# Kernel tuning notes

Hardware: AMD Instinct MI355X
Metric: run time of the kernel (lower is better)

The kernel has to match this reference:

```python
import jax, jax.numpy as jnp
import numpy as np

EPS = 1e-5
DILATIONS = (1, 2, 1, 2, 1, 2, 1, 2)   # 4 blocks x 2 layers, kernel_size=2
GCN_AT = {1: 0, 5: 1}                  # ChebConv applied before layers 1 and 5
N_NODES, T_IN, N_EDGES = 20000, 13, 200000
RC, DC, SC, EC, HORIZON = 32, 32, 256, 512, 12


def conv_1x1(x, W, b):
    # x: [N,C,T], W: [O,C] -> [N,O,T]
    return jnp.einsum('oc,nct->not', W, x) + b[None, :, None]


def conv_k2(x, W, b, d):
    # dilated conv, kernel=2, dilation=d. x: [N,C,T], W: [O,C,2] -> [N,O,T-d]
    y = jnp.einsum('oc,nct->not', W[:, :, 0], x[:, :, :-d]) \
        + jnp.einsum('oc,nct->not', W[:, :, 1], x[:, :, d:])
    return y + b[None, :, None]


def _batchnorm(x):
    # BatchNorm2d (train mode, gamma=1, beta=0); per-channel stats over (N, F=1, T)
    m = jnp.mean(x, axis=(0, 2), keepdims=True)
    v = jnp.var(x, axis=(0, 2), keepdims=True)
    return (x - m) / jnp.sqrt(v + EPS)


def _cheb(xf, edge_index, edge_attr, W0, W1, b):
    n = xf.shape[0]
    row, col = edge_index[0], edge_index[1]
    w = jnp.where(row == col, 0.0, edge_attr)               # remove_self_loops
    deg = jax.ops.segment_sum(w, row, num_segments=n)
    dinv = jnp.where(deg > 0, 1.0 / jnp.sqrt(jnp.where(deg > 0, deg, 1.0)), 0.0)
    norm = dinv[row] * w * dinv[col]                        # [E]
    tx1 = -jax.ops.segment_sum(norm[:, None] * xf[row], col, num_segments=n)
    return xf @ W0 + tx1 @ W1 + b


def _forward(x, edge_index, edge_attr, start_W, start_b, filter_W, filter_b,
             gate_W, gate_b, skip_W, skip_b, gcn0_W0, gcn0_W1, gcn0_b,
             gcn1_W0, gcn1_W1, gcn1_b, end1_W, end1_b, end2_W, end2_b):
    # instance norm over time (use_norm=True); means is detached in torch
    means = jax.lax.stop_gradient(jnp.mean(x, axis=1, keepdims=True))   # [N,1,1]
    xc = x - means
    stdev = jnp.sqrt(jnp.var(xc, axis=1, keepdims=True) + EPS)
    xc = xc / stdev
    h = xc[:, :, 0][:, None, :]                  # [N,1,13]  (F=1 dim folded away)
    h = conv_1x1(h, start_W, start_b)            # [N,32,13]; T == receptive_field, no pad
    gcns = ((gcn0_W0, gcn0_W1, gcn0_b), (gcn1_W0, gcn1_W1, gcn1_b))
    skip = None
    for i, d in enumerate(DILATIONS):
        if i in GCN_AT:
            n, c, t = h.shape
            W0, W1, b = gcns[GCN_AT[i]]
            h = _cheb(h.reshape(n, c * t), edge_index, edge_attr, W0, W1, b).reshape(n, c, t)
        residual = h
        f = jnp.tanh(conv_k2(residual, filter_W[i], filter_b[i], d))
        g = jax.nn.sigmoid(conv_k2(residual, gate_W[i], gate_b[i], d))
        h = f * g                                 # [N,32,t-d]
        s = conv_1x1(h, skip_W[i], skip_b[i])     # [N,256,t-d]
        skip = s if skip is None else s + skip[:, :, -s.shape[2]:]
        h = h + residual[:, :, -h.shape[2]:]      # residual add (residual_conv unused in source)
        h = _batchnorm(h)
    out = jax.nn.relu(skip)                       # [N,256,1]
    out = conv_1x1(out, end1_W, end1_b)           # [N,512,1]
    out = conv_1x1(out, end2_W, end2_b)           # [N,12,1]
    return out * stdev + means                    # de-normalize; broadcasts over horizon


def setup_inputs() -> dict:
    key = jax.random.key(0)
    ks = iter(jax.random.split(key, 32))
    def w(shape, scale=0.1):
        return jax.random.normal(next(ks), shape, dtype=jnp.float32) * scale
    return {
        'x': jax.random.normal(next(ks), (N_NODES, T_IN, 1), dtype=jnp.float32),
        'edge_index': jax.random.randint(next(ks), (2, N_EDGES), 0, N_NODES),
        'edge_attr': jax.random.uniform(next(ks), (N_EDGES,), dtype=jnp.float32),
        'start_W': w((RC, 1)), 'start_b': w((RC,)),
        'filter_W': w((8, DC, RC, 2)), 'filter_b': w((8, DC)),
        'gate_W': w((8, DC, RC, 2)), 'gate_b': w((8, DC)),
        'skip_W': w((8, SC, DC)), 'skip_b': w((8, SC)),
        'gcn0_W0': w((384, 384), 0.05), 'gcn0_W1': w((384, 384), 0.05), 'gcn0_b': w((384,)),
        'gcn1_W0': w((192, 192), 0.05), 'gcn1_W1': w((192, 192), 0.05), 'gcn1_b': w((192,)),
        'end1_W': w((EC, SC)), 'end1_b': w((EC,)),
        'end2_W': w((HORIZON, EC)), 'end2_b': w((HORIZON,)),
    }


def reference(x, edge_index, edge_attr, start_W, start_b, filter_W, filter_b,
              gate_W, gate_b, skip_W, skip_b, gcn0_W0, gcn0_W1, gcn0_b,
              gcn1_W0, gcn1_W1, gcn1_b, end1_W, end1_b, end2_W, end2_b):
    return _forward(x, edge_index, edge_attr, start_W, start_b, filter_W, filter_b,
                    gate_W, gate_b, skip_W, skip_b, gcn0_W0, gcn0_W1, gcn0_b,
                    gcn1_W0, gcn1_W1, gcn1_b, end1_W, end1_b, end2_W, end2_b)
```

## Files before the change

### kernel.cpp

```cpp
#include <hip/hip_runtime.h>
#include <math.h>

#define NN 20000
#define NE 200000
#define TT 13
#define NBLK 79

typedef short bf16x8 __attribute__((ext_vector_type(8)));
typedef float f32x4 __attribute__((ext_vector_type(4)));

__device__ inline unsigned short f2bf(float f){
  union{float f; unsigned u;} v; v.f = f;
  unsigned r = v.u + 0x7fffu + ((v.u >> 16) & 1u);
  return (unsigned short)(r >> 16);
}
__device__ inline float bf2f(unsigned short h){
  union{unsigned u; float f;} v; v.u = ((unsigned)h) << 16; return v.f;
}
__device__ inline float fsig(float x){ return __builtin_amdgcn_rcpf(1.f + __expf(-x)); }
__device__ inline float ftanh(float x){ return 2.f*__builtin_amdgcn_rcpf(1.f + __expf(-2.f*x)) - 1.f; }

__device__ inline void d_prepw2(const float* W0, const float* W1, const float* b,
    unsigned short* Wt, float* bPerm, int F, int Kp, int T, int idx){
  if(idx >= F*Kp) return;
// ... 26 lines not shown
  if(c == 0){
    float b = e2b[k];
    for(int o = 0; o < 512; o++) b += e2W[k*512+o]*e1b[o];
    bc[k] = b;
  }
}
__device__ inline void d_prepg(const float* fW, const float* fb,
    const float* gW, const float* gb, unsigned short* Wfrag, float* Bfrag, int idx){
  if(idx < 8*8*64*8){
    int j = idx & 7; int lane = (idx >> 3) & 63; int chunk = (idx >> 9) & 7; int layer = idx >> 12;
    int fg = chunk >> 2; int q = (chunk >> 1) & 1; int i = chunk & 1;
    int quad = lane >> 4, tcol = lane & 15;
    int cout = 16*i + tcol, cin = quad*8 + j;
    const float* W = fg ? gW : fW;
    Wfrag[idx] = f2bf(W[layer*2048 + cout*64 + cin*2 + q]);
  }
  if(idx < 8*64*4){
    int r = idx & 3; int lane = (idx >> 2) & 63; int layer = idx >> 8;
    int tcol = lane & 15;
    float v;
    if(r == 0)      v = fb[layer*32 + tcol];
    else if(r == 1) v = fb[layer*32 + 16 + tcol];
    else if(r == 2) v = gb[layer*32 + tcol];
    else            v = gb[layer*32 + 16 + tcol];
    Bfrag[idx] = v;
  }
}
__global__ __launch_bounds__(256) void k_prepall(
    const float* g0W0, const float* g0W1, const float* g0b,
    const float* g1W0, const float* g1W1, const float* g1b,
    const float* sW, const float* sb,
    const float* e1W, const float* e1b, const float* e2W, const float* e2b,
    const float* fW, const float* fb, const float* gW, const float* gb,
    unsigned short* Wt0, float* bP0, unsigned short* Wt1, float* bP1,
    unsigned short* Bwt, float* bias2, float* Wc, float* bc,
    unsigned short* Wfrag, float* Bfrag){
  int b = blockIdx.x, t = threadIdx.x;
  if(b < 1152)       d_prepw2(g0W0, g0W1, g0b, Wt0, bP0, 384, 768, 12, b*256 + t);
  else if(b < 1440)  d_prepw2(g1W0, g1W1, g1b, Wt1, bP1, 192, 384, 6, (b-1152)*256 + t);
  else if(b < 1696)  d_prep2(sW, sb, Bwt, bias2, (b-1440)*256 + t);
  else if(b < 1708)  d_comb(e1W, e1b, e2W, e2b, Wc, bc, (b-1696)*256 + t);
  else               d_prepg(fW, fb, gW, gb, Wfrag, Bfrag, (b-1708)*256 + t);
}

__global__ __launch_bounds__(256) void k_deg(const int* __restrict__ ei,
    const float* __restrict__ ea, float* __restrict__ deg){
  int e = blockIdx.x*256 + threadIdx.x;
  if(e >= NE) return;
  int r = ei[e], c = ei[NE+e];
  float w = (r==c) ? 0.f : ea[e];
  if(w != 0.f) atomicAdd(&deg[r], w);
}

__global__ __launch_bounds__(256) void k_dinv(float* __restrict__ deg){
  int n = blockIdx.x*256 + threadIdx.x;
  if(n >= NN) return;
  float d = deg[n];
  deg[n] = (d > 0.f) ? rsqrtf(d) : 0.f;
}

__global__ __launch_bounds__(256) void k_normcount(const int* __restrict__ ei,
    const float* __restrict__ ea, const float* __restrict__ dinv,
    float* __restrict__ nrm, int* __restrict__ cnt){
  int e = blockIdx.x*256 + threadIdx.x;
  if(e >= NE) return;
  int r = ei[e], c = ei[NE+e];
  float w = (r==c) ? 0.f : ea[e];
  float nv = dinv[r]*w*dinv[c];
  nrm[e] = nv;
  if(nv != 0.f) atomicAdd(&cnt[c], 1);
}

__global__ __launch_bounds__(256) void k_scanA(const int* __restrict__ cnt, int* __restrict__ bsum){
  int i = blockIdx.x*256 + threadIdx.x;
  int l = threadIdx.x & 63, w = threadIdx.x >> 6;
  int v = (i < NN) ? cnt[i] : 0;
#pragma unroll
  for(int off = 1; off < 64; off <<= 1) v += __shfl_xor(v, off);
  __shared__ int ws4[4];
  if(l == 0) ws4[w] = v;
  __syncthreads();
  if(threadIdx.x == 0) bsum[blockIdx.x] = ws4[0]+ws4[1]+ws4[2]+ws4[3];
}

__global__ __launch_bounds__(256) void k_scanC(const int* __restrict__ cnt,
    const int* __restrict__ bsum, int* __restrict__ rowptr, int* __restrict__ woff){
  __shared__ int sb[128];
  int t = threadIdx.x;
  if(t < 128) sb[t] = (t < NBLK) ? bsum[t] : 0;
  __syncthreads();
  for(int off = 1; off < 128; off <<= 1){
    int u = 0;
    if(t < 128 && t >= off) u = sb[t-off];
    __syncthreads();
    if(t < 128) sb[t] += u;
    __syncthreads();
  }
  int i = blockIdx.x*256 + t;
  int l = t & 63, w = t >> 6;
  int v = (i < NN) ? cnt[i] : 0;
  int x = v;
#pragma unroll
  for(int off = 1; off < 64; off <<= 1){
    int u = __shfl_up(x, off);
    if(l >= off) x += u;
  }
  __shared__ int wt[4];
  if(l == 63) wt[w] = x;
  __syncthreads();
  int wo = 0;
  for(int k = 0; k < w; k++) wo += wt[k];
  int bb = (blockIdx.x > 0) ? sb[blockIdx.x-1] : 0;
  int excl = bb + wo + x - v;
  if(i < NN){ rowptr[i] = excl; woff[i] = excl; }
  if(i == 0) rowptr[NN] = sb[NBLK-1];
}

__global__ __launch_bounds__(256) void k_place(const float* __restrict__ nrm,
    const int* __restrict__ ei, int* __restrict__ woff,
    int* __restrict__ rowArr, float* __restrict__ nrmArr){
  int e = blockIdx.x*256 + threadIdx.x;
  if(e >= NE) return;
  float nv = nrm[e];
  if(nv == 0.f) return;
  int c = ei[NE+e];
  int pos = atomicAdd(&woff[c], 1);
  rowArr[pos] = ei[e];
  nrmArr[pos] = nv;
}

__global__ void k_gather3(const unsigned short* __restrict__ h, int F, int F2,
    const float* __restrict__ bnstats, float cntInv,
    const int* __restrict__ rowArr, const float* __restrict__ nrmArr,
    const int* __restrict__ rowptr, unsigned short* __restrict__ tx1){
  __shared__ float bnm[32], bnv[32];
  __shared__ int srow[64];
  __shared__ float snrm[64];
  int tid = threadIdx.x;
  if(tid < 32){
    float s = 0.f, s2 = 0.f;
#pragma unroll
    for(int b = 0; b < 16; b++){ s += bnstats[b*64 + tid]; s2 += bnstats[b*64 + 32 + tid]; }
    float m = s*cntInv; float var = s2*cntInv - m*m;
    bnm[tid] = m; bnv[tid] = rsqrtf(var + 1e-5f);
  }
  __syncthreads();
  int node = blockIdx.x;
  int f2 = tid;
  int c0 = (2*f2) & 31;
  float m0 = bnm[c0], i0 = bnv[c0], m1 = bnm[c0+1], i1 = bnv[c0+1];
  int beg = rowptr[node], end = rowptr[node+1];
  float a0 = 0.f, a1 = 0.f;
  for(int base = beg; base < end; base += 64){
    int m = end - base; if(m > 64) m = 64;
    __syncthreads();
    if(tid < m){ srow[tid] = rowArr[base+tid]; snrm[tid] = nrmArr[base+tid]; }
    __syncthreads();
    if(f2 < F2){
      for(int j = 0; j < m; j++){
        unsigned u = *(const unsigned*)(h + (size_t)srow[j]*F + 2*f2);
        float nv = snrm[j];
        a0 += nv*(bf2f((unsigned short)(u & 0xffffu)) - m0)*i0;
        a1 += nv*(bf2f((unsigned short)(u >> 16)) - m1)*i1;
      }
    }
  }
  if(f2 < F2){
    unsigned outw = (unsigned)f2bf(-a0) | ((unsigned)f2bf(-a1) << 16);
    *(unsigned*)(tx1 + (size_t)node*F + 2*f2) = outw;
  }
}

template<bool BOUT>
__global__ __launch_bounds__(256) void k_gemm_gcn(
    const unsigned short* __restrict__ hSrc, const unsigned short* __restrict__ tx1,
    const unsigned short* __restrict__ Bt, const float* __restrict__ bias,
    const float* __restrict__ bnstats, float cntInv,
    void* __restrict__ Cv, int M, int N, int F){
  __shared__ unsigned short As[128*32];
  __shared__ unsigned short Bs[64*32];
  __shared__ float bnm[32], bnv[32];
  int tid = threadIdx.x;
  if(tid < 32){
    float s = 0.f, s2 = 0.f;
#pragma unroll
    for(int b = 0; b < 16; b++){ s += bnstats[b*64 + tid]; s2 += bnstats[b*64 + 32 + tid]; }
    float m = s*cntInv; float var = s2*cntInv - m*m;
    bnm[tid] = m; bnv[tid] = rsqrtf(var + 1e-5f);
  }
  __syncthreads();
  int w = tid >> 6, l = tid & 63, quad = l >> 4, tcol = l & 15;
  int m0 = blockIdx.x*128, n0 = blockIdx.y*64;
  int rw = (w & 1)*64, cw = (w >> 1)*32;
  int sr = tid >> 2, sc = (tid & 3)*8;
  float am[8], ai[8];
#pragma unroll
  for(int j = 0; j < 8; j++){ am[j] = bnm[sc+j]; ai[j] = bnv[sc+j]; }
  int K = 2*F;
  f32x4 acc[4][2];
#pragma unroll
  for(int i = 0; i < 4; i++)
#pragma unroll
    for(int j = 0; j < 2; j++) acc[i][j] = (f32x4){0.f,0.f,0.f,0.f};
  for(int k0 = 0; k0 < K; k0 += 32){
    uint4 a0r, a1r;
    if(k0 < F){
      uint4 r0 = *(const uint4*)(hSrc + (size_t)(m0 + sr)*F + k0 + sc);
      uint4 r1 = *(const uint4*)(hSrc + (size_t)(m0 + 64 + sr)*F + k0 + sc);
      unsigned short o0[8], o1[8];
      const unsigned short* p0 = (const unsigned short*)&r0;
      const unsigned short* p1 = (const unsigned short*)&r1;
#pragma unroll
      for(int j = 0; j < 8; j++){
        o0[j] = f2bf((bf2f(p0[j]) - am[j])*ai[j]);
        o1[j] = f2bf((bf2f(p1[j]) - am[j])*ai[j]);
      }
      a0r = *(const uint4*)o0; a1r = *(const uint4*)o1;
    } else {
      a0r = *(const uint4*)(tx1 + (size_t)(m0 + sr)*F + (k0-F) + sc);
      a1r = *(const uint4*)(tx1 + (size_t)(m0 + 64 + sr)*F + (k0-F) + sc);
    }
    uint4 b0 = *(const uint4*)(Bt + (size_t)(n0 + sr)*K + k0 + sc);
    __syncthreads();
    *(uint4*)(As + sr*32 + sc) = a0r;
    *(uint4*)(As + (64+sr)*32 + sc) = a1r;
    *(uint4*)(Bs + sr*32 + sc) = b0;
    __syncthreads();
    bf16x8 av[4], bv[2];
#pragma unroll
    for(int i = 0; i < 4; i++) av[i] = *(const bf16x8*)(As + (rw + 16*i + tcol)*32 + quad*8);
#pragma unroll
    for(int j = 0; j < 2; j++) bv[j] = *(const bf16x8*)(Bs + (cw + 16*j + tcol)*32 + quad*8);
#pragma unroll
    for(int i = 0; i < 4; i++)
#pragma unroll
      for(int j = 0; j < 2; j++)
        acc[i][j] = __builtin_amdgcn_mfma_f32_16x16x32_bf16(av[i], bv[j], acc[i][j], 0, 0, 0);
  }
#pragma unroll
  for(int i = 0; i < 4; i++){
#pragma unroll
    for(int j = 0; j < 2; j++){
      int col = n0 + cw + 16*j + tcol;
      float bb = bias[col];
#pragma unroll
      for(int r = 0; r < 4; r++){
        int row = m0 + rw + 16*i + quad*4 + r;
        if(row < M){
          float o = acc[i][j][r] + bb;
          if(BOUT) ((unsigned short*)Cv)[(size_t)row*N + col] = f2bf(o);
          else ((float*)Cv)[(size_t)row*N + col] = o;
        }
      }
    }
  }
}

template<bool BOUT>
__global__ __launch_bounds__(256) void k_gemm_bf16(const unsigned short* __restrict__ A,
    const unsigned short* __restrict__ Bt, const float* __restrict__ bias,
    void* __restrict__ Cv, int M, int N, int K){
  __shared__ unsigned short As[128*32];
  __shared__ unsigned short Bs[64*32];
  int tid = threadIdx.x;
  int w = tid >> 6, l = tid & 63, quad = l >> 4, tcol = l & 15;
  int m0 = blockIdx.x*128, n0 = blockIdx.y*64;
  int rw = (w & 1)*64, cw = (w >> 1)*32;
  int sr = tid >> 2, sc = (tid & 3)*8;
  f32x4 acc[4][2];
#pragma unroll
  for(int i = 0; i < 4; i++)
#pragma unroll
    for(int j = 0; j < 2; j++) acc[i][j] = (f32x4){0.f,0.f,0.f,0.f};
  for(int k0 = 0; k0 < K; k0 += 32){
    uint4 a0 = *(const uint4*)(A + (size_t)(m0 + sr)*K + k0 + sc);
    uint4 a1 = *(const uint4*)(A + (size_t)(m0 + 64 + sr)*K + k0 + sc);
    uint4 b0 = *(const uint4*)(Bt + (size_t)(n0 + sr)*K + k0 + sc);
    __syncthreads();
    *(uint4*)(As + sr*32 + sc) = a0;
    *(uint4*)(As + (64+sr)*32 + sc) = a1;
    *(uint4*)(Bs + sr*32 + sc) = b0;
    __syncthreads();
    bf16x8 av[4], bv[2];
#pragma unroll
    for(int i = 0; i < 4; i++) av[i] = *(const bf16x8*)(As + (rw + 16*i + tcol)*32 + quad*8);
#pragma unroll
    for(int j = 0; j < 2; j++) bv[j] = *(const bf16x8*)(Bs + (cw + 16*j + tcol)*32 + quad*8);
#pragma unroll
    for(int i = 0; i < 4; i++)
#pragma unroll
      for(int j = 0; j < 2; j++)
        acc[i][j] = __builtin_amdgcn_mfma_f32_16x16x32_bf16(av[i], bv[j], acc[i][j], 0, 0, 0);
  }
#pragma unroll
  for(int i = 0; i < 4; i++){
#pragma unroll
    for(int j = 0; j < 2; j++){
      int col = n0 + cw + 16*j + tcol;
      float bb = bias[col];
#pragma unroll
      for(int r = 0; r < 4; r++){
        int row = m0 + rw + 16*i + quad*4 + r;
        if(row < M){
          float o = acc[i][j][r] + bb;
          if(BOUT) ((unsigned short*)Cv)[(size_t)row*N + col] = f2bf(o);
          else ((float*)Cv)[(size_t)row*N + col] = o;
        }
      }
    }
  }
}

__global__ __launch_bounds__(256,3) void k_fused0nb(
    const float* __restrict__ x, const float* __restrict__ startW, const float* __restrict__ startb,
    const unsigned short* __restrict__ Wfrag, const float* __restrict__ Bfrag,
    unsigned short* __restrict__ glcat, unsigned short* __restrict__ hOut,
    float* __restrict__ stdev, float* __restrict__ means,
    float* __restrict__ bnstats){
  __shared__ float xs[40][14];
  __shared__ float swl[32], sbl[32];
  __shared__ unsigned short bufB[40*12*40];
  __shared__ float bnred[64];
  int tid = threadIdx.x;
  int w = tid >> 6, l = tid & 63, quad = l >> 4, tcol = l & 15;
  int base = blockIdx.x*40;
  for(int j = tid; j < 520; j += 256){ int n = j/13, t = j - n*13; xs[n][t] = x[(size_t)(base+n)*13 + t]; }
  if(tid < 32){ swl[tid] = startW[tid]; sbl[tid] = startb[tid]; }
  if(tid < 64) bnred[tid] = 0.f;
  __syncthreads();
  if(tid < 40){
    float s = 0.f;
#pragma unroll
    for(int t = 0; t < 13; t++) s += xs[tid][t];
    float m = s*(1.0f/13.f);
    float s2 = 0.f;
#pragma unroll
    for(int t = 0; t < 13; t++){ float d = xs[tid][t]-m; s2 += d*d; }
    float sd = sqrtf(s2*(1.0f/13.f) + 1e-5f);
    float inv = 1.0f/sd;
    means[base+tid] = m; stdev[base+tid] = sd;
#pragma unroll
    for(int t = 0; t < 13; t++) xs[tid][t] = (xs[tid][t]-m)*inv;
  }
  __syncthreads();
  bf16x8 bwf[2][2], bwg[2][2];
#pragma unroll
  for(int q = 0; q < 2; q++)
#pragma unroll
    for(int i = 0; i < 2; i++){
      bwf[q][i] = *(const bf16x8*)(Wfrag + ((q*2+i)*64 + l)*8);
      bwg[q][i] = *(const bf16x8*)(Wfrag + ((4 + q*2+i)*64 + l)*8);
    }
  float4 bv4 = *(const float4*)(Bfrag + l*4);
  float fbv[2] = {bv4.x, bv4.y}, gbv[2] = {bv4.z, bv4.w};
  float sw8[8], sb8[8], swc[2], sbc[2];
#pragma unroll
  for(int j = 0; j < 8; j++){ sw8[j] = swl[quad*8+j]; sb8[j] = sbl[quad*8+j]; }
#pragma unroll
  for(int i = 0; i < 2; i++){ swc[i] = swl[16*i+tcol]; sbc[i] = sbl[16*i+tcol]; }
  float sAc[2] = {0.f,0.f}, s2Ac[2] = {0.f,0.f};
  int tr = (tcol < 12) ? tcol : 0;
  for(int p = 0; p < 5; p++){
    int slA = w*10 + 2*p, slB = slA + 1;
// ... 169 lines not shown
      agA[i] = __builtin_amdgcn_mfma_f32_16x16x32_bf16(aA0, bwg[0][i], agA[i], 0,0,0);
      agB[i] = __builtin_amdgcn_mfma_f32_16x16x32_bf16(aB0, bwg[0][i], agB[i], 0,0,0);
      agA[i] = __builtin_amdgcn_mfma_f32_16x16x32_bf16(aA1, bwg[1][i], agA[i], 0,0,0);
      agB[i] = __builtin_amdgcn_mfma_f32_16x16x32_bf16(aB1, bwg[1][i], agB[i], 0,0,0);
    }
#pragma unroll
    for(int i=0;i<2;i++){
      int cout = 16*i + tcol;
#pragma unroll
      for(int r=0;r<4;r++){
        int t = quad*4 + r;
        if(t < TOUT){
          float fA = afA[i][r] + fbv[i];
          float gA = agA[i][r] + gbv[i];
          float fB = afB[i][r] + fbv[i];
          float gB = agB[i][r] + gbv[i];
          float gatedA = ftanh(fA)*fsig(gA);
          float gatedB = ftanh(fB)*fsig(gB);
          if(t == TOUT-1){
            gl[(size_t)nA*256 + cout] = f2bf(gatedA);
            gl[(size_t)nB*256 + cout] = f2bf(gatedB);
          }
          float oA = gatedA + bf2f(hwA[(t+D)*RS + cout]);
          float oB = gatedB + bf2f(hwB[(t+D)*RS + cout]);
          if(WRITEH){ howA[t*RS + cout] = f2bf(oA); howB[t*RS + cout] = f2bf(oB); }
          if(STATS){ sA[i] += oA + oB; s2A[i] += oA*oA + oB*oB; }
        }
      }
    }
    if(WRITEH && l < TOUT*4){
      int to = l >> 2, cb2 = (l & 3)*8;
      *(uint4*)(hOut + (size_t)nA*TOUT*32 + to*32 + cb2) = *(const uint4*)(howA + to*RS + cb2);
      *(uint4*)(hOut + (size_t)nB*TOUT*32 + to*32 + cb2) = *(const uint4*)(howB + to*RS + cb2);
    }
  }
  if(STATS){
#pragma unroll
    for(int i=0;i<2;i++){
      sA[i]  += __shfl_xor(sA[i], 16);  sA[i]  += __shfl_xor(sA[i], 32);
      s2A[i] += __shfl_xor(s2A[i], 16); s2A[i] += __shfl_xor(s2A[i], 32);
    }
    if(l < 16){
#pragma unroll
      for(int i=0;i<2;i++){
        atomicAdd(&bnred[16*i + l], sA[i]);
        atomicAdd(&bnred[32 + 16*i + l], s2A[i]);
      }
    }
    __syncthreads();
    if(tid < 64) atomicAdd(&bnOut[(blockIdx.x & 15)*64 + tid], bnred[tid]);
  }
}

__global__ __launch_bounds__(256) void k_final(const float* __restrict__ skip,
    const float* __restrict__ Wc, const float* __restrict__ bc,
    const float* __restrict__ stdev, const float* __restrict__ means,
    float* __restrict__ out){
  __shared__ float wsm[3072];
  __shared__ float bcs[12];
  int tid = threadIdx.x;
  for(int j = tid; j < 3072; j += 256){
    int c = j / 12, k = j - c*12;
    wsm[c*12 + k] = Wc[k*256 + c];
  }
  if(tid < 12) bcs[tid] = bc[tid];
  __syncthreads();
  int idx = blockIdx.x*256 + tid;
  if(idx >= NN*12) return;
  int n = idx / 12, k = idx - n*12;
  const float* sr = skip + (size_t)n*256;
  float acc = bcs[k];
#pragma unroll 8
  for(int c = 0; c < 256; c++) acc += wsm[c*12 + k]*fmaxf(sr[c], 0.f);
  out[idx] = acc*stdev[n] + means[n];
}

extern "C" void kernel_launch(void* const* d_in, const int* in_sizes, int n_in,
                              void* d_out, int out_size, void* d_ws, size_t ws_size,
                              hipStream_t stream) {
  const float* x      = (const float*)d_in[0];
  const int*   ei     = (const int*)  d_in[1];
  const float* ea     = (const float*)d_in[2];
  const float* startW = (const float*)d_in[3];
  const float* startb = (const float*)d_in[4];
  const float* fW     = (const float*)d_in[5];
  const float* fb     = (const float*)d_in[6];
  const float* gW     = (const float*)d_in[7];
  const float* gb     = (const float*)d_in[8];
  const float* sW     = (const float*)d_in[9];
  const float* sb     = (const float*)d_in[10];
  const float* g0W0   = (const float*)d_in[11];
  const float* g0W1   = (const float*)d_in[12];
  const float* g0b    = (const float*)d_in[13];
  const float* g1W0   = (const float*)d_in[14];
  const float* g1W1   = (const float*)d_in[15];
  const float* g1b    = (const float*)d_in[16];
  const float* e1W    = (const float*)d_in[17];
  const float* e1b    = (const float*)d_in[18];
  const float* e2W    = (const float*)d_in[19];
  const float* e2b    = (const float*)d_in[20];
  float* out = (float*)d_out;
  float* ws  = (float*)d_ws;

  const int MP = 20096;
  size_t o = 0;
  float* hAf = ws + o; o += (size_t)NN*208;
  float* hBf = ws + o; o += (size_t)NN*208;
  unsigned short* hA = (unsigned short*)hAf;
  unsigned short* hB = (unsigned short*)hBf;
  unsigned short* tx1   = (unsigned short*)(ws + o); o += (size_t)MP*192;
  unsigned short* glcat = (unsigned short*)(ws + o); o += (size_t)MP*128;
  unsigned short* Wt0 = (unsigned short*)(ws + o); o += 147456;
  unsigned short* Wt1 = (unsigned short*)(ws + o); o += 36864;
  unsigned short* Bwt = (unsigned short*)(ws + o); o += 32768;
  unsigned short* Wfrag = (unsigned short*)(ws + o); o += 16384;
  float* Bfrag = ws + o; o += 2048;
  float* bP0   = ws + o; o += 384;
  float* bP1   = ws + o; o += 192;
  float* bias2 = ws + o; o += 256;
  float* Wc    = ws + o; o += 3072;
  float* bc    = ws + o; o += 16;
  float* stdev = ws + o; o += NN;
  float* means = ws + o; o += NN;
  float* deg   = ws + o; o += NN;
  int*   cnt   = (int*)(ws + o); o += NN;
  float* bnstats = ws + o; o += 8*1024;
  float* normb = ws + o; o += NE;
  int*   rowArr = (int*)(ws + o); o += NE;
  float* nrmArr = ws + o; o += NE;
  int*   rowptr = (int*)(ws + o); o += NN + 4;
  int*   woff   = (int*)(ws + o); o += NN;
  int*   bsum   = (int*)(ws + o); o += NBLK + 4;
  float* skipb  = hAf;

  hipMemsetAsync(deg, 0, (size_t)(2*NN + 8*1024)*sizeof(float), stream);
  k_prepall<<<1836, 256, 0, stream>>>(g0W0, g0W1, g0b, g1W0, g1W1, g1b,
      sW, sb, e1W, e1b, e2W, e2b, fW, fb, gW, gb,
      Wt0, bP0, Wt1, bP1, Bwt, bias2, Wc, bc, Wfrag, Bfrag);
  k_deg<<<(NE+255)/256, 256, 0, stream>>>(ei, ea, deg);
  k_dinv<<<(NN+255)/256, 256, 0, stream>>>(deg);
  k_normcount<<<(NE+255)/256, 256, 0, stream>>>(ei, ea, deg, normb, cnt);
  k_scanA<<<NBLK, 256, 0, stream>>>(cnt, bsum);
  k_scanC<<<NBLK, 256, 0, stream>>>(cnt, bsum, rowptr, woff);
  k_place<<<(NE+255)/256, 256, 0, stream>>>(normb, ei, woff, rowArr, nrmArr);

  const int GB = 1280;
  k_fused0nb<<<500, 256, 0, stream>>>(x, startW, startb, Wfrag, Bfrag, glcat, hB,
      stdev, means, bnstats);
  k_gather3<<<NN, 192, 0, stream>>>(hB, 384, 192, bnstats, 1.f/(NN*12.f),
      rowArr, nrmArr, rowptr, tx1);
  { dim3 g(MP/128, 384/64);
    k_gemm_gcn<true><<<g, 256, 0, stream>>>(hB, tx1, Wt0, bP0, bnstats, 1.f/(NN*12.f),
        hA, NN, 384, 384); }
  k_gated5<2,12,10,false,true,true><<<GB,256,0,stream>>>(hA, hB, glcat+32,
      bnstats, bnstats+1*1024, Wfrag, Bfrag, 1, 0.f);
  k_gated5<1,10,9,true,true,true><<<GB,256,0,stream>>>(hB, hA, glcat+64,
      bnstats+1*1024, bnstats+2*1024, Wfrag, Bfrag, 2, 1.f/(NN*10.f));
  k_gated5<2,9,7,true,true,true><<<GB,256,0,stream>>>(hA, hB, glcat+96,
      bnstats+2*1024, bnstats+3*1024, Wfrag, Bfrag, 3, 1.f/(NN*9.f));
  k_gated5<1,7,6,true,true,true><<<GB,256,0,stream>>>(hB, hA, glcat+128,
      bnstats+3*1024, bnstats+4*1024, Wfrag, Bfrag, 4, 1.f/(NN*7.f));
  k_gather3<<<NN, 128, 0, stream>>>(hA, 192, 96, bnstats+4*1024, 1.f/(NN*6.f),
      rowArr, nrmArr, rowptr, tx1);
  { dim3 g(MP/128, 192/64);
    k_gemm_gcn<true><<<g, 256, 0, stream>>>(hA, tx1, Wt1, bP1, bnstats+4*1024, 1.f/(NN*6.f),
        hB, NN, 192, 192); }
  k_gated5<2,6,4,false,true,true><<<GB,256,0,stream>>>(hB, hA, glcat+160,
      bnstats, bnstats+5*1024, Wfrag, Bfrag, 5, 0.f);
  k_gated5<1,4,3,true,true,true><<<GB,256,0,stream>>>(hA, hB, glcat+192,
      bnstats+5*1024, bnstats+6*1024, Wfrag, Bfrag, 6, 1.f/(NN*4.f));
  k_gated5<2,3,1,true,false,false><<<GB,256,0,stream>>>(hB, nullptr, glcat+224,
      bnstats+6*1024, bnstats+7*1024, Wfrag, Bfrag, 7, 1.f/(NN*3.f));

  { dim3 g(MP/128, 256/64);
    k_gemm_bf16<false><<<g, 256, 0, stream>>>(glcat, Bwt, bias2, skipb, NN, 256, 256); }
  k_final<<<((NN*12)+255)/256, 256, 0, stream>>>(skipb, Wc, bc, stdev, means, out);
}
```

Before: 432.8 us.

## Fuse GCN GEMM with following gated layer and skip GEMM with final head

Replaces the standalone ChebConv GEMM and the next gated TCN layer with one kernel. It keeps the 32-node GCN output tile in shared memory, runs the dilated filter/gate MFMAs on it and accumulates the batch-norm statistics there. It also fuses the skip GEMM with the ReLU and end-projection head so the fp32 skip buffer is never written out, and folds the dinv kernel into normcount. This removes intermediate global round-trips and several launches. In exchange the fused GCN kernel uses narrow 32-row tiles that reload the full weight matrix per block, with large shared memory and possibly lower occupancy.

```diff
diff --git a/kernel.cpp b/kernel.cpp
--- a/kernel.cpp
+++ b/kernel.cpp
@@ -102,21 +102,17 @@
   if(w != 0.f) atomicAdd(&deg[r], w);
 }
 
-__global__ __launch_bounds__(256) void k_dinv(float* __restrict__ deg){
-  int n = blockIdx.x*256 + threadIdx.x;
-  if(n >= NN) return;
-  float d = deg[n];
-  deg[n] = (d > 0.f) ? rsqrtf(d) : 0.f;
-}
-
 __global__ __launch_bounds__(256) void k_normcount(const int* __restrict__ ei,
-    const float* __restrict__ ea, const float* __restrict__ dinv,
+    const float* __restrict__ ea, const float* __restrict__ deg,
     float* __restrict__ nrm, int* __restrict__ cnt){
   int e = blockIdx.x*256 + threadIdx.x;
   if(e >= NE) return;
   int r = ei[e], c = ei[NE+e];
   float w = (r==c) ? 0.f : ea[e];
-  float nv = dinv[r]*w*dinv[c];
+  float dr = deg[r], dc = deg[c];
+  float ir = (dr > 0.f) ? rsqrtf(dr) : 0.f;
+  float ic = (dc > 0.f) ? rsqrtf(dc) : 0.f;
+  float nv = ir*w*ic;
   nrm[e] = nv;
   if(nv != 0.f) atomicAdd(&cnt[c], 1);
 }
@@ -221,16 +217,22 @@
   }
 }
 
-template<bool BOUT>
-__global__ __launch_bounds__(256) void k_gemm_gcn(
+template<int F,int TIN,int TOUT,int D,int NCT>
+__global__ __launch_bounds__(256) void k_gcn_gated(
     const unsigned short* __restrict__ hSrc, const unsigned short* __restrict__ tx1,
-    const unsigned short* __restrict__ Bt, const float* __restrict__ bias,
+    const unsigned short* __restrict__ Bt, const float* __restrict__ biasP,
     const float* __restrict__ bnstats, float cntInv,
-    void* __restrict__ Cv, int M, int N, int F){
-  __shared__ unsigned short As[128*32];
-  __shared__ unsigned short Bs[64*32];
+    const unsigned short* __restrict__ Wfrag, const float* __restrict__ Bfrag, int layer,
+    unsigned short* __restrict__ gl, unsigned short* __restrict__ hOut,
+    float* __restrict__ bnOut){
+  constexpr int RS = 40;
+  constexpr int SH = (F*32 > 32*TIN*RS) ? F*32 : 32*TIN*RS;
+  __shared__ unsigned short shm[SH];
+  __shared__ unsigned short As[32*32];
   __shared__ float bnm[32], bnv[32];
+  __shared__ float bnred[64];
   int tid = threadIdx.x;
+  int w = tid >> 6, l = tid & 63, quad = l >> 4, tcol = l & 15;
   if(tid < 32){
     float s = 0.f, s2 = 0.f;
 #pragma unroll
@@ -238,127 +240,155 @@
     float m = s*cntInv; float var = s2*cntInv - m*m;
     bnm[tid] = m; bnv[tid] = rsqrtf(var + 1e-5f);
   }
-  __syncthreads();
-  int w = tid >> 6, l = tid & 63, quad = l >> 4, tcol = l & 15;
-  int m0 = blockIdx.x*128, n0 = blockIdx.y*64;
-  int rw = (w & 1)*64, cw = (w >> 1)*32;
-  int sr = tid >> 2, sc = (tid & 3)*8;
+  if(tid < 64) bnred[tid] = 0.f;
+  __syncthreads();
+  int m0 = blockIdx.x*32;
   float am[8], ai[8];
-#pragma unroll
-  for(int j = 0; j < 8; j++){ am[j] = bnm[sc+j]; ai[j] = bnv[sc+j]; }
-  int K = 2*F;
-  f32x4 acc[4][2];
-#pragma unroll
-  for(int i = 0; i < 4; i++)
-#pragma unroll
-    for(int j = 0; j < 2; j++) acc[i][j] = (f32x4){0.f,0.f,0.f,0.f};
+  {
+    int off8 = (tid & 3)*8;
+#pragma unroll
+    for(int j = 0; j < 8; j++){ am[j] = bnm[off8+j]; ai[j] = bnv[off8+j]; }
+  }
+  constexpr int NB4 = F*4/256;
+  f32x4 acc[2][NCT];
+#pragma unroll
+  for(int i = 0; i < 2; i++)
+#pragma unroll
+    for(int j = 0; j < NCT; j++) acc[i][j] = (f32x4){0.f,0.f,0.f,0.f};
+  const int K = 2*F;
   for(int k0 = 0; k0 < K; k0 += 32){
-    uint4 a0r, a1r;
-    if(k0 < F){
-      uint4 r0 = *(const uint4*)(hSrc + (size_t)(m0 + sr)*F + k0 + sc);
-      uint4 r1 = *(const uint4*)(hSrc + (size_t)(m0 + 64 + sr)*F + k0 + sc);
-      unsigned short o0[8], o1[8];
-      const unsigned short* p0 = (const unsigned short*)&r0;
-      const unsigned short* p1 = (const unsigned short*)&r1;
-#pragma unroll
-      for(int j = 0; j < 8; j++){
-        o0[j] = f2bf((bf2f(p0[j]) - am[j])*ai[j]);
-        o1[j] = f2bf((bf2f(p1[j]) - am[j])*ai[j]);
+    uint4 a4 = {0,0,0,0};
+    if(tid < 128){
+      int row = tid >> 2, off = (tid & 3)*8;
+      if(k0 < F){
+        uint4 r0 = *(const uint4*)(hSrc + (size_t)(m0+row)*F + k0 + off);
+        unsigned short o0[8];
+        const unsigned short* p0 = (const unsigned short*)&r0;
+#pragma unroll
+        for(int j = 0; j < 8; j++) o0[j] = f2bf((bf2f(p0[j]) - am[j])*ai[j]);
+        a4 = *(const uint4*)o0;
+      } else {
+        a4 = *(const uint4*)(tx1 + (size_t)(m0+row)*F + (k0-F) + off);
       }
-      a0r = *(const uint4*)o0; a1r = *(const uint4*)o1;
-    } else {
-      a0r = *(const uint4*)(tx1 + (size_t)(m0 + sr)*F + (k0-F) + sc);
-      a1r = *(const uint4*)(tx1 + (size_t)(m0 + 64 + sr)*F + (k0-F) + sc);
-    }
-    uint4 b0 = *(const uint4*)(Bt + (size_t)(n0 + sr)*K + k0 + sc);
+    }
+    uint4 b4[NB4];
+#pragma unroll
+    for(int it = 0; it < NB4; it++){
+      int idx = tid + 256*it;
+      b4[it] = *(const uint4*)(Bt + (size_t)(idx>>2)*K + k0 + (idx&3)*8);
+    }
     __syncthreads();
-    *(uint4*)(As + sr*32 + sc) = a0r;
-    *(uint4*)(As + (64+sr)*32 + sc) = a1r;
-    *(uint4*)(Bs + sr*32 + sc) = b0;
+    if(tid < 128) *(uint4*)(As + (tid>>2)*32 + (tid&3)*8) = a4;
+#pragma unroll
+    for(int it = 0; it < NB4; it++){
+      int idx = tid + 256*it;
+      *(uint4*)(shm + (idx>>2)*32 + (idx&3)*8) = b4[it];
+    }
     __syncthreads();
-    bf16x8 av[4], bv[2];
-#pragma unroll
-    for(int i = 0; i < 4; i++) av[i] = *(const bf16x8*)(As + (rw + 16*i + tcol)*32 + quad*8);
-#pragma unroll
-    for(int j = 0; j < 2; j++) bv[j] = *(const bf16x8*)(Bs + (cw + 16*j + tcol)*32 + quad*8);
-#pragma unroll
-    for(int i = 0; i < 4; i++)
-#pragma unroll
-      for(int j = 0; j < 2; j++)
+    bf16x8 av[2], bv[NCT];
+#pragma unroll
+    for(int i = 0; i < 2; i++) av[i] = *(const bf16x8*)(As + (16*i + tcol)*32 + quad*8);
+#pragma unroll
+    for(int j = 0; j < NCT; j++) bv[j] = *(const bf16x8*)(shm + ((w*NCT + j)*16 + tcol)*32 + quad*8);
+#pragma unroll
+    for(int i = 0; i < 2; i++)
+#pragma unroll
+      for(int j = 0; j < NCT; j++)
         acc[i][j] = __builtin_amdgcn_mfma_f32_16x16x32_bf16(av[i], bv[j], acc[i][j], 0, 0, 0);
   }
-#pragma unroll
-  for(int i = 0; i < 4; i++){
-#pragma unroll
-    for(int j = 0; j < 2; j++){
-      int col = n0 + cw + 16*j + tcol;
-      float bb = bias[col];
+  __syncthreads();
+  unsigned short* hs = shm;
+#pragma unroll
+  for(int i = 0; i < 2; i++)
+#pragma unroll
+    for(int j = 0; j < NCT; j++){
+      int col = (w*NCT + j)*16 + tcol;
+      float bb = biasP[col];
+      int t = col >> 5, c = col & 31;
 #pragma unroll
       for(int r = 0; r < 4; r++){
-        int row = m0 + rw + 16*i + quad*4 + r;
-        if(row < M){
-          float o = acc[i][j][r] + bb;
-          if(BOUT) ((unsigned short*)Cv)[(size_t)row*N + col] = f2bf(o);
-          else ((float*)Cv)[(size_t)row*N + col] = o;
+        int node = 16*i + quad*4 + r;
+        hs[node*(TIN*RS) + t*RS + c] = f2bf(acc[i][j][r] + bb);
+      }
+    }
+  __syncthreads();
+  const unsigned short* wfr = Wfrag + layer*4096;
+  bf16x8 bwf[2][2], bwg[2][2];
+#pragma unroll
+  for(int q = 0; q < 2; q++)
+#pragma unroll
+    for(int i = 0; i < 2; i++){
+      bwf[q][i] = *(const bf16x8*)(wfr + ((q*2+i)*64 + l)*8);
+      bwg[q][i] = *(const bf16x8*)(wfr + ((4 + q*2+i)*64 + l)*8);
+    }
+  float4 bq = *(const float4*)(Bfrag + layer*256 + l*4);
+  float fbv[2] = {bq.x, bq.y}, gbv[2] = {bq.z, bq.w};
+  int tr = (tcol < TOUT) ? tcol : 0;
+  float sAc[2] = {0.f,0.f}, s2Ac[2] = {0.f,0.f};
+  for(int p = 0; p < 4; p++){
+    int slA = w*8 + 2*p, slB = slA + 1;
+    const unsigned short* inA = hs + slA*(TIN*RS);
+    const unsigned short* inB = hs + slB*(TIN*RS);
+    bf16x8 aA0 = *(const bf16x8*)(inA + tr*RS + quad*8);
+    bf16x8 aA1 = *(const bf16x8*)(inA + (tr+D)*RS + quad*8);
+    bf16x8 aB0 = *(const bf16x8*)(inB + tr*RS + quad*8);
+    bf16x8 aB1 = *(const bf16x8*)(inB + (tr+D)*RS + quad*8);
+    f32x4 afA[2], agA[2], afB[2], agB[2];
+#pragma unroll
+    for(int i = 0; i < 2; i++){
+      afA[i] = (f32x4){0.f,0.f,0.f,0.f}; agA[i] = afA[i];
+      afB[i] = afA[i]; agB[i] = afA[i];
+    }
+#pragma unroll
+    for(int i = 0; i < 2; i++){
+      afA[i] = __builtin_amdgcn_mfma_f32_16x16x32_bf16(aA0, bwf[0][i], afA[i], 0,0,0);
+      afB[i] = __builtin_amdgcn_mfma_f32_16x16x32_bf16(aB0, bwf[0][i], afB[i], 0,0,0);
+      afA[i] = __builtin_amdgcn_mfma_f32_16x16x32_bf16(aA1, bwf[1][i], afA[i], 0,0,0);
+      afB[i] = __builtin_amdgcn_mfma_f32_16x16x32_bf16(aB1, bwf[1][i], afB[i], 0,0,0);
+      agA[i] = __builtin_amdgcn_mfma_f32_16x16x32_bf16(aA0, bwg[0][i], agA[i], 0,0,0);
+      agB[i] = __builtin_amdgcn_mfma_f32_16x16x32_bf16(aB0, bwg[0][i], agB[i], 0,0,0);
+      agA[i] = __builtin_amdgcn_mfma_f32_16x16x32_bf16(aA1, bwg[1][i], agA[i], 0,0,0);
+      agB[i] = __builtin_amdgcn_mfma_f32_16x16x32_bf16(aB1, bwg[1][i], agB[i], 0,0,0);
+    }
+    int nA = m0 + slA, nB = m0 + slB;
+#pragma unroll
+    for(int i = 0; i < 2; i++){
+      int cout = 16*i + tcol;
+#pragma unroll
+      for(int r = 0; r < 4; r++){
+        int t = quad*4 + r;
+        if(t < TOUT){
+          float fA = afA[i][r] + fbv[i], gA = agA[i][r] + gbv[i];
+          float fB = afB[i][r] + fbv[i], gB = agB[i][r] + gbv[i];
+          float gatA = ftanh(fA)*fsig(gA);
+          float gatB = ftanh(fB)*fsig(gB);
+          if(t == TOUT-1){
+            gl[(size_t)nA*256 + cout] = f2bf(gatA);
+            gl[(size_t)nB*256 + cout] = f2bf(gatB);
+          }
+          float oA = gatA + bf2f(inA[(t+D)*RS + cout]);
+          float oB = gatB + bf2f(inB[(t+D)*RS + cout]);
+          hOut[(size_t)nA*(TOUT*32) + t*32 + cout] = f2bf(oA);
+          hOut[(size_t)nB*(TOUT*32) + t*32 + cout] = f2bf(oB);
+          sAc[i] += oA + oB; s2Ac[i] += oA*oA + oB*oB;
         }
       }
     }
   }
-}
-
-template<bool BOUT>
-__global__ __launch_bounds__(256) void k_gemm_bf16(const unsigned short* __restrict__ A,
-    const unsigned short* __restrict__ Bt, const float* __restrict__ bias,
-    void* __restrict__ Cv, int M, int N, int K){
-  __shared__ unsigned short As[128*32];
-  __shared__ unsigned short Bs[64*32];
-  int tid = threadIdx.x;
-  int w = tid >> 6, l = tid & 63, quad = l >> 4, tcol = l & 15;
-  int m0 = blockIdx.x*128, n0 = blockIdx.y*64;
-  int rw = (w & 1)*64, cw = (w >> 1)*32;
-  int sr = tid >> 2, sc = (tid & 3)*8;
-  f32x4 acc[4][2];
-#pragma unroll
-  for(int i = 0; i < 4; i++)
-#pragma unroll
-    for(int j = 0; j < 2; j++) acc[i][j] = (f32x4){0.f,0.f,0.f,0.f};
-  for(int k0 = 0; k0 < K; k0 += 32){
-    uint4 a0 = *(const uint4*)(A + (size_t)(m0 + sr)*K + k0 + sc);
-    uint4 a1 = *(const uint4*)(A + (size_t)(m0 + 64 + sr)*K + k0 + sc);
-    uint4 b0 = *(const uint4*)(Bt + (size_t)(n0 + sr)*K + k0 + sc);
-    __syncthreads();
-    *(uint4*)(As + sr*32 + sc) = a0;
-    *(uint4*)(As + (64+sr)*32 + sc) = a1;
-    *(uint4*)(Bs + sr*32 + sc) = b0;
-    __syncthreads();
-    bf16x8 av[4], bv[2];
-#pragma unroll
-    for(int i = 0; i < 4; i++) av[i] = *(const bf16x8*)(As + (rw + 16*i + tcol)*32 + quad*8);
-#pragma unroll
-    for(int j = 0; j < 2; j++) bv[j] = *(const bf16x8*)(Bs + (cw + 16*j + tcol)*32 + quad*8);
-#pragma unroll
-    for(int i = 0; i < 4; i++)
-#pragma unroll
-      for(int j = 0; j < 2; j++)
-        acc[i][j] = __builtin_amdgcn_mfma_f32_16x16x32_bf16(av[i], bv[j], acc[i][j], 0, 0, 0);
-  }
-#pragma unroll
-  for(int i = 0; i < 4; i++){
-#pragma unroll
-    for(int j = 0; j < 2; j++){
-      int col = n0 + cw + 16*j + tcol;
-      float bb = bias[col];
-#pragma unroll
-      for(int r = 0; r < 4; r++){
-        int row = m0 + rw + 16*i + quad*4 + r;
-        if(row < M){
-          float o = acc[i][j][r] + bb;
-          if(BOUT) ((unsigned short*)Cv)[(size_t)row*N + col] = f2bf(o);
-          else ((float*)Cv)[(size_t)row*N + col] = o;
-        }
-      }
-    }
-  }
+#pragma unroll
+  for(int i = 0; i < 2; i++){
+    sAc[i]  += __shfl_xor(sAc[i], 16);  sAc[i]  += __shfl_xor(sAc[i], 32);
+    s2Ac[i] += __shfl_xor(s2Ac[i], 16); s2Ac[i] += __shfl_xor(s2Ac[i], 32);
+  }
+  if(l < 16){
+#pragma unroll
+    for(int i = 0; i < 2; i++){
+      atomicAdd(&bnred[16*i + l], sAc[i]);
+      atomicAdd(&bnred[32 + 16*i + l], s2Ac[i]);
+    }
+  }
+  __syncthreads();
+  if(tid < 64) atomicAdd(&bnOut[(blockIdx.x & 15)*64 + tid], bnred[tid]);
 }
 
 __global__ __launch_bounds__(256,3) void k_fused0nb(
@@ -634,27 +664,86 @@
   }
 }
 
-__global__ __launch_bounds__(256) void k_final(const float* __restrict__ skip,
+__global__ __launch_bounds__(256) void k_skip_final(
+    const unsigned short* __restrict__ A, const unsigned short* __restrict__ Bt,
+    const float* __restrict__ bias2,
     const float* __restrict__ Wc, const float* __restrict__ bc,
     const float* __restrict__ stdev, const float* __restrict__ means,
     float* __restrict__ out){
+  constexpr int RSK = 264;
+  __shared__ unsigned short pool[64*RSK];
   __shared__ float wsm[3072];
   __shared__ float bcs[12];
+  unsigned short* As = pool;
+  unsigned short* Bs = pool + 64*32;
   int tid = threadIdx.x;
+  int w = tid >> 6, l = tid & 63, quad = l >> 4, tcol = l & 15;
   for(int j = tid; j < 3072; j += 256){
     int c = j / 12, k = j - c*12;
     wsm[c*12 + k] = Wc[k*256 + c];
   }
   if(tid < 12) bcs[tid] = bc[tid];
-  __syncthreads();
-  int idx = blockIdx.x*256 + tid;
-  if(idx >= NN*12) return;
-  int n = idx / 12, k = idx - n*12;
-  const float* sr = skip + (size_t)n*256;
-  float acc = bcs[k];
-#pragma unroll 8
-  for(int c = 0; c < 256; c++) acc += wsm[c*12 + k]*fmaxf(sr[c], 0.f);
-  out[idx] = acc*stdev[n] + means[n];
+  int m0 = blockIdx.x*64;
+  f32x4 acc[4][4];
+#pragma unroll
+  for(int i = 0; i < 4; i++)
+#pragma unroll
+    for(int j = 0; j < 4; j++) acc[i][j] = (f32x4){0.f,0.f,0.f,0.f};
+  for(int k0 = 0; k0 < 256; k0 += 32){
+    int row = tid >> 2, off = (tid & 3)*8;
+    uint4 a4 = *(const uint4*)(A + (size_t)(m0+row)*256 + k0 + off);
+    uint4 b4[4];
+#pragma unroll
+    for(int it = 0; it < 4; it++){
+      int idx = tid + 256*it;
+      b4[it] = *(const uint4*)(Bt + (size_t)(idx>>2)*256 + k0 + (idx&3)*8);
+    }
+    __syncthreads();
+    *(uint4*)(As + row*32 + off) = a4;
+#pragma unroll
+    for(int it = 0; it < 4; it++){
+      int idx = tid + 256*it;
+      *(uint4*)(Bs + (idx>>2)*32 + (idx&3)*8) = b4[it];
+    }
+    __syncthreads();
+    bf16x8 av[4], bv[4];
+#pragma unroll
+    for(int i = 0; i < 4; i++) av[i] = *(const bf16x8*)(As + (16*i + tcol)*32 + quad*8);
+#pragma unroll
+    for(int j = 0; j < 4; j++) bv[j] = *(const bf16x8*)(Bs + ((w*4 + j)*16 + tcol)*32 + quad*8);
+#pragma unroll
+    for(int i = 0; i < 4; i++)
+#pragma unroll
+      for(int j = 0; j < 4; j++)
+        acc[i][j] = __builtin_amdgcn_mfma_f32_16x16x32_bf16(av[i], bv[j], acc[i][j], 0, 0, 0);
+  }
+  __syncthreads();
+#pragma unroll
+  for(int i = 0; i < 4; i++)
+#pragma unroll
+    for(int j = 0; j < 4; j++){
+      int col = (w*4 + j)*16 + tcol;
+      float bb = bias2[col];
+#pragma unroll
+      for(int r = 0; r < 4; r++){
+        int node = 16*i + quad*4 + r;
+        pool[node*RSK + col] = f2bf(fmaxf(acc[i][j][r] + bb, 0.f));
+      }
+    }
+  __syncthreads();
+  int n = tid & 63, kb = (tid >> 6)*3;
+  float a0 = bcs[kb], a1 = bcs[kb+1], a2 = bcs[kb+2];
+  for(int c = 0; c < 256; c++){
+    float s = bf2f(pool[n*RSK + c]);
+    a0 += s*wsm[c*12 + kb]; a1 += s*wsm[c*12 + kb+1]; a2 += s*wsm[c*12 + kb+2];
+  }
+  int gn = m0 + n;
+  if(gn < NN){
+    float sd = stdev[gn], mn = means[gn];
+    out[gn*12 + kb]   = a0*sd + mn;
+    out[gn*12 + kb+1] = a1*sd + mn;
+    out[gn*12 + kb+2] = a2*sd + mn;
+  }
 }
 
 extern "C" void kernel_launch(void* const* d_in, const int* in_sizes, int n_in,
@@ -713,14 +802,12 @@
   int*   rowptr = (int*)(ws + o); o += NN + 4;
   int*   woff   = (int*)(ws + o); o += NN;
   int*   bsum   = (int*)(ws + o); o += NBLK + 4;
-  float* skipb  = hAf;
 
   hipMemsetAsync(deg, 0, (size_t)(2*NN + 8*1024)*sizeof(float), stream);
   k_prepall<<<1836, 256, 0, stream>>>(g0W0, g0W1, g0b, g1W0, g1W1, g1b,
       sW, sb, e1W, e1b, e2W, e2b, fW, fb, gW, gb,
       Wt0, bP0, Wt1, bP1, Bwt, bias2, Wc, bc, Wfrag, Bfrag);
   k_deg<<<(NE+255)/256, 256, 0, stream>>>(ei, ea, deg);
-  k_dinv<<<(NN+255)/256, 256, 0, stream>>>(deg);
   k_normcount<<<(NE+255)/256, 256, 0, stream>>>(ei, ea, deg, normb, cnt);
   k_scanA<<<NBLK, 256, 0, stream>>>(cnt, bsum);
   k_scanC<<<NBLK, 256, 0, stream>>>(cnt, bsum, rowptr, woff);
@@ -731,30 +818,23 @@
       stdev, means, bnstats);
   k_gather3<<<NN, 192, 0, stream>>>(hB, 384, 192, bnstats, 1.f/(NN*12.f),
       rowArr, nrmArr, rowptr, tx1);
-  { dim3 g(MP/128, 384/64);
-    k_gemm_gcn<true><<<g, 256, 0, stream>>>(hB, tx1, Wt0, bP0, bnstats, 1.f/(NN*12.f),
-        hA, NN, 384, 384); }
-  k_gated5<2,12,10,false,true,true><<<GB,256,0,stream>>>(hA, hB, glcat+32,
-      bnstats, bnstats+1*1024, Wfrag, Bfrag, 1, 0.f);
-  k_gated5<1,10,9,true,true,true><<<GB,256,0,stream>>>(hB, hA, glcat+64,
+  k_gcn_gated<384,12,10,2,6><<<NN/32, 256, 0, stream>>>(hB, tx1, Wt0, bP0,
+      bnstats, 1.f/(NN*12.f), Wfrag, Bfrag, 1, glcat+32, hA, bnstats+1*1024);
+  k_gated5<1,10,9,true,true,true><<<GB,256,0,stream>>>(hA, hB, glcat+64,
       bnstats+1*1024, bnstats+2*1024, Wfrag, Bfrag, 2, 1.f/(NN*10.f));
-  k_gated5<2,9,7,true,true,true><<<GB,256,0,stream>>>(hA, hB, glcat+96,
+  k_gated5<2,9,7,true,true,true><<<GB,256,0,stream>>>(hB, hA, glcat+96,
       bnstats+2*1024, bnstats+3*1024, Wfrag, Bfrag, 3, 1.f/(NN*9.f));
-  k_gated5<1,7,6,true,true,true><<<GB,256,0,stream>>>(hB, hA, glcat+128,
+  k_gated5<1,7,6,true,true,true><<<GB,256,0,stream>>>(hA, hB, glcat+128,
       bnstats+3*1024, bnstats+4*1024, Wfrag, Bfrag, 4, 1.f/(NN*7.f));
-  k_gather3<<<NN, 128, 0, stream>>>(hA, 192, 96, bnstats+4*1024, 1.f/(NN*6.f),
+  k_gather3<<<NN, 128, 0, stream>>>(hB, 192, 96, bnstats+4*1024, 1.f/(NN*6.f),
       rowArr, nrmArr, rowptr, tx1);
-  { dim3 g(MP/128, 192/64);
-    k_gemm_gcn<true><<<g, 256, 0, stream>>>(hA, tx1, Wt1, bP1, bnstats+4*1024, 1.f/(NN*6.f),
-        hB, NN, 192, 192); }
-  k_gated5<2,6,4,false,true,true><<<GB,256,0,stream>>>(hB, hA, glcat+160,
-      bnstats, bnstats+5*1024, Wfrag, Bfrag, 5, 0.f);
+  k_gcn_gated<192,6,4,2,3><<<NN/32, 256, 0, stream>>>(hB, tx1, Wt1, bP1,
+      bnstats+4*1024, 1.f/(NN*6.f), Wfrag, Bfrag, 5, glcat+160, hA, bnstats+5*1024);
   k_gated5<1,4,3,true,true,true><<<GB,256,0,stream>>>(hA, hB, glcat+192,
       bnstats+5*1024, bnstats+6*1024, Wfrag, Bfrag, 6, 1.f/(NN*4.f));
   k_gated5<2,3,1,true,false,false><<<GB,256,0,stream>>>(hB, nullptr, glcat+224,
       bnstats+6*1024, bnstats+7*1024, Wfrag, Bfrag, 7, 1.f/(NN*3.f));
 
-  { dim3 g(MP/128, 256/64);
-    k_gemm_bf16<false><<<g, 256, 0, stream>>>(glcat, Bwt, bias2, skipb, NN, 256, 256); }
-  k_final<<<((NN*12)+255)/256, 256, 0, stream>>>(skipb, Wc, bc, stdev, means, out);
-}
+  k_skip_final<<<(NN+63)/64, 256, 0, stream>>>(glcat, Bwt, bias2, Wc, bc,
+      stdev, means, out);
+}
```

After: 520.7 us. 1.2x slower.

## Fuse skip GEMM with final projection and fold dinv into normcount

Applied to the files above, without the earlier changes.

Replaces the separate skip-channel bf16 GEMM and the final end-projection kernel with one kernel. It computes the 64x256 skip tile with MFMA, applies bias and ReLU, stages the result in LDS as bf16, and then applies the combined 256->12 projection plus de-normalization. This avoids writing and re-reading the fp32 skip buffer (20000x256) through global memory. It also removes the k_dinv launch by computing rsqrt of the degree inline per edge, and rounds the skip activations to bf16 before the final projection, which may slightly change accuracy.

```diff
diff --git a/kernel.cpp b/kernel.cpp
--- a/kernel.cpp
+++ b/kernel.cpp
@@ -102,21 +102,17 @@
   if(w != 0.f) atomicAdd(&deg[r], w);
 }
 
-__global__ __launch_bounds__(256) void k_dinv(float* __restrict__ deg){
-  int n = blockIdx.x*256 + threadIdx.x;
-  if(n >= NN) return;
-  float d = deg[n];
-  deg[n] = (d > 0.f) ? rsqrtf(d) : 0.f;
-}
-
 __global__ __launch_bounds__(256) void k_normcount(const int* __restrict__ ei,
-    const float* __restrict__ ea, const float* __restrict__ dinv,
+    const float* __restrict__ ea, const float* __restrict__ deg,
     float* __restrict__ nrm, int* __restrict__ cnt){
   int e = blockIdx.x*256 + threadIdx.x;
   if(e >= NE) return;
   int r = ei[e], c = ei[NE+e];
   float w = (r==c) ? 0.f : ea[e];
-  float nv = dinv[r]*w*dinv[c];
+  float dr = deg[r], dc = deg[c];
+  float ir = (dr > 0.f) ? rsqrtf(dr) : 0.f;
+  float ic = (dc > 0.f) ? rsqrtf(dc) : 0.f;
+  float nv = ir*w*ic;
   nrm[e] = nv;
   if(nv != 0.f) atomicAdd(&cnt[c], 1);
 }
@@ -274,61 +270,6 @@
     __syncthreads();
     *(uint4*)(As + sr*32 + sc) = a0r;
     *(uint4*)(As + (64+sr)*32 + sc) = a1r;
-    *(uint4*)(Bs + sr*32 + sc) = b0;
-    __syncthreads();
-    bf16x8 av[4], bv[2];
-#pragma unroll
-    for(int i = 0; i < 4; i++) av[i] = *(const bf16x8*)(As + (rw + 16*i + tcol)*32 + quad*8);
-#pragma unroll
-    for(int j = 0; j < 2; j++) bv[j] = *(const bf16x8*)(Bs + (cw + 16*j + tcol)*32 + quad*8);
-#pragma unroll
-    for(int i = 0; i < 4; i++)
-#pragma unroll
-      for(int j = 0; j < 2; j++)
-        acc[i][j] = __builtin_amdgcn_mfma_f32_16x16x32_bf16(av[i], bv[j], acc[i][j], 0, 0, 0);
-  }
-#pragma unroll
-  for(int i = 0; i < 4; i++){
-#pragma unroll
-    for(int j = 0; j < 2; j++){
-      int col = n0 + cw + 16*j + tcol;
-      float bb = bias[col];
-#pragma unroll
-      for(int r = 0; r < 4; r++){
-        int row = m0 + rw + 16*i + quad*4 + r;
-        if(row < M){
-          float o = acc[i][j][r] + bb;
-          if(BOUT) ((unsigned short*)Cv)[(size_t)row*N + col] = f2bf(o);
-          else ((float*)Cv)[(size_t)row*N + col] = o;
-        }
-      }
-    }
-  }
-}
-
-template<bool BOUT>
-__global__ __launch_bounds__(256) void k_gemm_bf16(const unsigned short* __restrict__ A,
-    const unsigned short* __restrict__ Bt, const float* __restrict__ bias,
-    void* __restrict__ Cv, int M, int N, int K){
-  __shared__ unsigned short As[128*32];
-  __shared__ unsigned short Bs[64*32];
-  int tid = threadIdx.x;
-  int w = tid >> 6, l = tid & 63, quad = l >> 4, tcol = l & 15;
-  int m0 = blockIdx.x*128, n0 = blockIdx.y*64;
-  int rw = (w & 1)*64, cw = (w >> 1)*32;
-  int sr = tid >> 2, sc = (tid & 3)*8;
-  f32x4 acc[4][2];
-#pragma unroll
-  for(int i = 0; i < 4; i++)
-#pragma unroll
-    for(int j = 0; j < 2; j++) acc[i][j] = (f32x4){0.f,0.f,0.f,0.f};
-  for(int k0 = 0; k0 < K; k0 += 32){
-    uint4 a0 = *(const uint4*)(A + (size_t)(m0 + sr)*K + k0 + sc);
-    uint4 a1 = *(const uint4*)(A + (size_t)(m0 + 64 + sr)*K + k0 + sc);
-    uint4 b0 = *(const uint4*)(Bt + (size_t)(n0 + sr)*K + k0 + sc);
-    __syncthreads();
-    *(uint4*)(As + sr*32 + sc) = a0;
-    *(uint4*)(As + (64+sr)*32 + sc) = a1;
     *(uint4*)(Bs + sr*32 + sc) = b0;
     __syncthreads();
     bf16x8 av[4], bv[2];
@@ -634,27 +575,86 @@
   }
 }
 
-__global__ __launch_bounds__(256) void k_final(const float* __restrict__ skip,
+__global__ __launch_bounds__(256) void k_skip_final(
+    const unsigned short* __restrict__ A, const unsigned short* __restrict__ Bt,
+    const float* __restrict__ bias2,
     const float* __restrict__ Wc, const float* __restrict__ bc,
     const float* __restrict__ stdev, const float* __restrict__ means,
     float* __restrict__ out){
+  constexpr int RSK = 264;
+  __shared__ unsigned short pool[64*RSK];
   __shared__ float wsm[3072];
   __shared__ float bcs[12];
+  unsigned short* As = pool;
+  unsigned short* Bs = pool + 64*32;
   int tid = threadIdx.x;
+  int w = tid >> 6, l = tid & 63, quad = l >> 4, tcol = l & 15;
   for(int j = tid; j < 3072; j += 256){
     int c = j / 12, k = j - c*12;
     wsm[c*12 + k] = Wc[k*256 + c];
   }
   if(tid < 12) bcs[tid] = bc[tid];
-  __syncthreads();
-  int idx = blockIdx.x*256 + tid;
-  if(idx >= NN*12) return;
-  int n = idx / 12, k = idx - n*12;
-  const float* sr = skip + (size_t)n*256;
-  float acc = bcs[k];
-#pragma unroll 8
-  for(int c = 0; c < 256; c++) acc += wsm[c*12 + k]*fmaxf(sr[c], 0.f);
-  out[idx] = acc*stdev[n] + means[n];
+  int m0 = blockIdx.x*64;
+  f32x4 acc[4][4];
+#pragma unroll
+  for(int i = 0; i < 4; i++)
+#pragma unroll
+    for(int j = 0; j < 4; j++) acc[i][j] = (f32x4){0.f,0.f,0.f,0.f};
+  for(int k0 = 0; k0 < 256; k0 += 32){
+    int row = tid >> 2, off = (tid & 3)*8;
+    uint4 a4 = *(const uint4*)(A + (size_t)(m0+row)*256 + k0 + off);
+    uint4 b4[4];
+#pragma unroll
+    for(int it = 0; it < 4; it++){
+      int idx = tid + 256*it;
+      b4[it] = *(const uint4*)(Bt + (size_t)(idx>>2)*256 + k0 + (idx&3)*8);
+    }
+    __syncthreads();
+    *(uint4*)(As + row*32 + off) = a4;
+#pragma unroll
+    for(int it = 0; it < 4; it++){
+      int idx = tid + 256*it;
+      *(uint4*)(Bs + (idx>>2)*32 + (idx&3)*8) = b4[it];
+    }
+    __syncthreads();
+    bf16x8 av[4], bv[4];
+#pragma unroll
+    for(int i = 0; i < 4; i++) av[i] = *(const bf16x8*)(As + (16*i + tcol)*32 + quad*8);
+#pragma unroll
+    for(int j = 0; j < 4; j++) bv[j] = *(const bf16x8*)(Bs + ((w*4 + j)*16 + tcol)*32 + quad*8);
+#pragma unroll
+    for(int i = 0; i < 4; i++)
+#pragma unroll
+      for(int j = 0; j < 4; j++)
+        acc[i][j] = __builtin_amdgcn_mfma_f32_16x16x32_bf16(av[i], bv[j], acc[i][j], 0, 0, 0);
+  }
+  __syncthreads();
+#pragma unroll
+  for(int i = 0; i < 4; i++)
+#pragma unroll
+    for(int j = 0; j < 4; j++){
+      int col = (w*4 + j)*16 + tcol;
+      float bb = bias2[col];
+#pragma unroll
+      for(int r = 0; r < 4; r++){
+        int node = 16*i + quad*4 + r;
+        pool[node*RSK + col] = f2bf(fmaxf(acc[i][j][r] + bb, 0.f));
+      }
+    }
+  __syncthreads();
+  int n = tid & 63, kb = (tid >> 6)*3;
+  float a0 = bcs[kb], a1 = bcs[kb+1], a2 = bcs[kb+2];
+  for(int c = 0; c < 256; c++){
+    float s = bf2f(pool[n*RSK + c]);
+    a0 += s*wsm[c*12 + kb]; a1 += s*wsm[c*12 + kb+1]; a2 += s*wsm[c*12 + kb+2];
+  }
+  int gn = m0 + n;
+  if(gn < NN){
+    float sd = stdev[gn], mn = means[gn];
+    out[gn*12 + kb]   = a0*sd + mn;
+    out[gn*12 + kb+1] = a1*sd + mn;
+    out[gn*12 + kb+2] = a2*sd + mn;
+  }
 }
 
 extern "C" void kernel_launch(void* const* d_in, const int* in_sizes, int n_in,
@@ -713,14 +713,12 @@
   int*   rowptr = (int*)(ws + o); o += NN + 4;
   int*   woff   = (int*)(ws + o); o += NN;
   int*   bsum   = (int*)(ws + o); o += NBLK + 4;
-  float* skipb  = hAf;
 
   hipMemsetAsync(deg, 0, (size_t)(2*NN + 8*1024)*sizeof(float), stream);
   k_prepall<<<1836, 256, 0, stream>>>(g0W0, g0W1, g0b, g1W0, g1W1, g1b,
       sW, sb, e1W, e1b, e2W, e2b, fW, fb, gW, gb,
       Wt0, bP0, Wt1, bP1, Bwt, bias2, Wc, bc, Wfrag, Bfrag);
   k_deg<<<(NE+255)/256, 256, 0, stream>>>(ei, ea, deg);
-  k_dinv<<<(NN+255)/256, 256, 0, stream>>>(deg);
   k_normcount<<<(NE+255)/256, 256, 0, stream>>>(ei, ea, deg, normb, cnt);
   k_scanA<<<NBLK, 256, 0, stream>>>(cnt, bsum);
   k_scanC<<<NBLK, 256, 0, stream>>>(cnt, bsum, rowptr, woff);
@@ -754,7 +752,6 @@
   k_gated5<2,3,1,true,false,false><<<GB,256,0,stream>>>(hB, nullptr, glcat+224,
       bnstats+6*1024, bnstats+7*1024, Wfrag, Bfrag, 7, 1.f/(NN*3.f));
 
-  { dim3 g(MP/128, 256/64);
-    k_gemm_bf16<false><<<g, 256, 0, stream>>>(glcat, Bwt, bias2, skipb, NN, 256, 256); }
-  k_final<<<((NN*12)+255)/256, 256, 0, stream>>>(skipb, Wc, bc, stdev, means, out);
-}
+  k_skip_final<<<(NN+63)/64, 256, 0, stream>>>(glcat, Bwt, bias2, Wc, bc,
+      stdev, means, out);
+}
```

After: 429.8 us. Within noise of the previous version (-0.7%).
